# Optimization experiments

Measured on AMD Instinct MI355X. Metric: run time of the kernel, lower is better.

Reference implementation:

```python
import jax, jax.numpy as jnp
import numpy as np

# Straight-through sign binarization: forward -> {-1, +1}, backward -> identity
@jax.custom_vjp
def binarize(x):
    return jnp.where(x >= 0, jnp.ones_like(x), -jnp.ones_like(x))

def _bin_fwd(x):
    return binarize(x), None

def _bin_bwd(res, g):
    return (g,)

binarize.defvjp(_bin_fwd, _bin_bwd)

BATCH = 16384
IN_SIZE = 1025   # must be 2**n + 1
HIDDEN = 1025    # must be 2**n + 1

def setup_inputs() -> dict:
    key = jax.random.key(0)
    k0, k1, k2, k3 = jax.random.split(key, 4)
    # weight init scale per reset_parameters: sqrt(1.5/(in+out)) uniform
    s = float(np.sqrt(1.5 / (IN_SIZE + HIDDEN)))
    return {
        "x": jax.random.normal(k0, (BATCH, IN_SIZE), dtype=jnp.float32),
        "W0": jax.random.uniform(k1, (HIDDEN, IN_SIZE), jnp.float32, -s, s),
        "W1": jax.random.uniform(k2, (HIDDEN, HIDDEN), jnp.float32, -s, s),
        "W2": jax.random.uniform(k3, (1, HIDDEN), jnp.float32, -s, s),
    }

def reference(x, W0, W1, W2):
    # x: [B, IN_SIZE]; weights stored [out, in] (nn.Linear convention), no bias
    h = x.reshape(-1, IN_SIZE)
    for W in (W0, W1, W2):
        lin = h @ binarize(W).T          # float GEMM against +/-1 weights
        h = binarize(lin)                # sign activation
    # num_classes == 2 path: to_boolean maps {-1,+1} -> {0,1}, then squeeze
    out = (h + 1.0) * 0.5
    return out.squeeze(-1)               # [B]
```

## Files before the change

### kernel.cpp

```cpp
#include <hip/hip_runtime.h>
#include <cstdint>

typedef unsigned long long u64;
typedef unsigned short ushort_t;
typedef __attribute__((ext_vector_type(8))) short short8;
typedef __attribute__((ext_vector_type(4))) float f32x4;

#define B_TOTAL 16384
#define K_DIM   1025
#define O_DIM   1025
#define NWORDS  17
#define NKT     34
#define NFRAG   72
#define A_BYTES 8192
#define B_BYTES 73728
#define STEP_BYTES (A_BYTES + B_BYTES)
#define L23_ROWS 16

__device__ __forceinline__ ushort_t f2bf_rne(float f) {
  unsigned u = __float_as_uint(f);
  return (ushort_t)((u + 0x7fffu + ((u >> 16) & 1u)) >> 16);
}

__device__ __forceinline__ void gload16(const ushort_t* g, char* l) {
  __builtin_amdgcn_global_load_lds(
      (const __attribute__((address_space(1))) void*)g,
      (__attribute__((address_space(3))) void*)l, 16, 0, 0);
}

__global__ __launch_bounds__(256) void pack_all_kernel(const float* __restrict__ W0,
                                                       const float* __restrict__ W1,
                                                       const float* __restrict__ W2,
                                                       u64* __restrict__ w0b,
                                                       u64* __restrict__ w1b,
                                                       u64* __restrict__ w2b,
                                                       unsigned* cnt) {
  __shared__ unsigned char by[136];
  const int row = blockIdx.x, t = threadIdx.x;
  if (row == 0 && t == 0) *cnt = 0;
  const float* src; u64* dst; int o;
  if (row < O_DIM)           { src = W0; dst = w0b; o = row; }
  else if (row < 2 * O_DIM)  { src = W1; dst = w1b; o = row - O_DIM; }
  else                       { src = W2; dst = w2b; o = 0; }
  if (t < 136) {
    const float* wr = src + (size_t)o * K_DIM;
    unsigned m = 0;
#pragma unroll
    for (int j = 0; j < 8; ++j) {
      int k = t * 8 + j;
      bool pos = (k < K_DIM) ? (wr[k] >= 0.0f) : true;
      m |= (unsigned)pos << j;
    }
    by[t] = (unsigned char)m;
  }
  __syncthreads();
  if (t < NWORDS) {
    u64 word = 0;
#pragma unroll
    for (int q = 0; q < 8; ++q) word |= (u64)by[t * 8 + q] << (8 * q);
    dst[(size_t)o * NWORDS + t] = word;
  }
}

__global__ __launch_bounds__(256) void prep_sbf_kernel(const float* __restrict__ w0,
                                                       ushort_t* __restrict__ sbf) {
  const int t = threadIdx.x;
  const int f = blockIdx.x * 4 + (t >> 6);
  const int lane = t & 63;
  const int kt = f / NFRAG, nf = f % NFRAG;
  const int o = nf * 16 + (lane & 15);
  const int kbase = kt * 32 + (lane >> 4) * 8;
  short8 sv;
#pragma unroll
  for (int j = 0; j < 8; ++j) {
    int k = kbase + j;
    short v = 0;
    if (o < O_DIM && k < K_DIM)
      v = (short)((w0[(size_t)o * K_DIM + k] >= 0.0f) ? 0x3F80 : 0xBF80);
    sv[j] = v;
  }
  *(short8*)&sbf[(size_t)f * 512 + lane * 8] = sv;
}

__global__ __launch_bounds__(256) void prep_xf_kernel(const float* __restrict__ x,
                                                      ushort_t* __restrict__ xf,
                                                      float* __restrict__ errb) {
  const int p = blockIdx.x, t = threadIdx.x;
  const int mf = t >> 6, lane = t & 63;
  const int lr = lane & 15, lg = lane >> 4;
  const int brow = p * 64 + mf * 16 + lr;
  const float* xr = x + (size_t)brow * K_DIM;
  float s = 0.0f;
  for (int kt = 0; kt < NKT; ++kt) {
    const int kbase = kt * 32 + lg * 8;
    float v[8];
    if (kbase + 8 <= K_DIM) {
      float4 a = *(const float4*)(xr + kbase);
      float4 b = *(const float4*)(xr + kbase + 4);
      v[0]=a.x; v[1]=a.y; v[2]=a.z; v[3]=a.w; v[4]=b.x; v[5]=b.y; v[6]=b.z; v[7]=b.w;
    } else {
#pragma unroll
      for (int j = 0; j < 8; ++j) v[j] = (kbase + j < K_DIM) ? xr[kbase + j] : 0.0f;
    }
    short8 hi, lo;
#pragma unroll
    for (int j = 0; j < 8; ++j) {
      s += fabsf(v[j]);
      ushort_t h = f2bf_rne(v[j]);
      float hf = __uint_as_float((unsigned)h << 16);
      ushort_t l = f2bf_rne(v[j] - hf);
      hi[j] = (short)h; lo[j] = (short)l;
    }
    size_t base = ((size_t)(p * NKT + kt) * 8 + mf) * 512 + lane * 8;
    *(short8*)&xf[base] = hi;
    *(short8*)&xf[base + 4 * 512] = lo;
  }
  s += __shfl_xor(s, 16, 64);
  s += __shfl_xor(s, 32, 64);
  if (lg == 0) errb[brow] = s * (1.02f / 65536.0f) + 0.125f;
}

__global__ __launch_bounds__(512, 2) void l1_gemm_kernel(
    const ushort_t* __restrict__ xf, const ushort_t* __restrict__ sbf,
    const float* __restrict__ errb, u64* __restrict__ h1b,
    unsigned* __restrict__ cnt, unsigned* __restrict__ list, unsigned cap) {
  extern __shared__ char smem[];
  const int p = blockIdx.x;
  const int t = threadIdx.x;
  const int wave = t >> 6, lane = t & 63;
  const int lr = lane & 15, lg = lane >> 4;
  const int b0 = p * 64;
  const int obase = wave * 144;

  const ushort_t* gA = xf + (size_t)p * NKT * (A_BYTES / 2);

  f32x4 acc[4][9];
#pragma unroll
  for (int mf = 0; mf < 4; ++mf)
#pragma unroll
    for (int nfl = 0; nfl < 9; ++nfl)
#pragma unroll
      for (int c = 0; c < 4; ++c) acc[mf][nfl][c] = 0.0f;

#define STAGE(BUFI, KT)                                                        \
  {                                                                            \
    char* dbuf = smem + (BUFI) * STEP_BYTES;                                   \
    _Pragma("unroll")                                                          \
    for (int i = 0; i < 10; ++i) {                                             \
      int s = wave * 10 + i;                                                   \
      const ushort_t* g = (s < 8)                                              \
          ? gA + (KT) * (A_BYTES / 2) + s * 512 + lane * 8                     \
          : sbf + (size_t)(KT) * (B_BYTES / 2) + (s - 8) * 512 + lane * 8;     \
      gload16(g, dbuf + s * 1024);                                             \
    }                                                                          \
  }

  STAGE(0, 0);
  __syncthreads();
  int cur = 0;
  for (int kt = 0; kt < NKT; ++kt) {
    if (kt + 1 < NKT) STAGE(cur ^ 1, kt + 1);
    const ushort_t* A = (const ushort_t*)(smem + cur * STEP_BYTES);
    const ushort_t* Bf = A + A_BYTES / 2;
    short8 ah[4], al[4];
#pragma unroll
    for (int mf = 0; mf < 4; ++mf) {
      ah[mf] = *(const short8*)&A[mf * 512 + lane * 8];
      al[mf] = *(const short8*)&A[(4 + mf) * 512 + lane * 8];
    }
#pragma unroll
    for (int nfl = 0; nfl < 9; ++nfl) {
      short8 bv = *(const short8*)&Bf[(wave * 9 + nfl) * 512 + lane * 8];
#pragma unroll
      for (int mf = 0; mf < 4; ++mf) {
        acc[mf][nfl] = __builtin_amdgcn_mfma_f32_16x16x32_bf16(ah[mf], bv, acc[mf][nfl], 0, 0, 0);
        acc[mf][nfl] = __builtin_amdgcn_mfma_f32_16x16x32_bf16(al[mf], bv, acc[mf][nfl], 0, 0, 0);
      }
    }
    __syncthreads();
    cur ^= 1;
  }
#undef STAGE

  unsigned char* bits = (unsigned char*)smem;
  int* scan = (int*)(smem + 73728);

  float eb[4][4];
#pragma unroll
  for (int mf = 0; mf < 4; ++mf)
#pragma unroll
    for (int rg = 0; rg < 4; ++rg) eb[mf][rg] = errb[b0 + mf * 16 + lg * 4 + rg];

  int myCnt = 0;
#pragma unroll
  for (int mf = 0; mf < 4; ++mf)
#pragma unroll
    for (int nfl = 0; nfl < 9; ++nfl)
#pragma unroll
      for (int rg = 0; rg < 4; ++rg) {
        int bl = mf * 16 + lg * 4 + rg;
        int o  = obase + nfl * 16 + lr;
        float lin = acc[mf][nfl][rg];
        bits[bl * 1152 + o] = (lin >= 0.0f) ? 1u : 0u;
        myCnt += (int)((o < O_DIM) && (fabsf(lin) <= eb[mf][rg]));
      }

  int incl = myCnt;
#pragma unroll
  for (int d = 1; d < 64; d <<= 1) {
    int v = __shfl_up(incl, d, 64);
    if (lane >= d) incl += v;
  }
  if (lane == 63) scan[wave] = incl;
  __syncthreads();
  if (t == 0) {
    int run = 0;
#pragma unroll
    for (int i = 0; i < 8; ++i) { int c = scan[i]; scan[8 + i] = run; run += c; }
    scan[16] = (run > 0) ? (int)atomicAdd(cnt, (unsigned)run) : 0;
  }
  __syncthreads();

  {
    int off = scan[16] + scan[8 + wave] + incl - myCnt;
#pragma unroll
    for (int mf = 0; mf < 4; ++mf)
#pragma unroll
      for (int nfl = 0; nfl < 9; ++nfl)
#pragma unroll
        for (int rg = 0; rg < 4; ++rg) {
          int o = obase + nfl * 16 + lr;
          float lin = acc[mf][nfl][rg];
          if ((o < O_DIM) && (fabsf(lin) <= eb[mf][rg])) {
            int b = b0 + mf * 16 + lg * 4 + rg;
            unsigned abit = (lin >= 0.0f) ? 1u : 0u;
            if ((unsigned)off < cap)
              list[off] = ((unsigned)b << 12) | ((unsigned)o << 1) | abit;
            ++off;
          }
        }
  }

  for (int task = t; task < 64 * NWORDS; task += 512) {
    int row = task / NWORDS, w = task % NWORDS;
    u64 word = 0;
#pragma unroll
    for (int q = 0; q < 8; ++q) {
      u64 v = *(const u64*)&bits[row * 1152 + w * 64 + q * 8];
#pragma unroll
      for (int m = 0; m < 8; ++m)
        word |= ((v >> (8 * m)) & 1ull) << (q * 8 + m);
    }
    int rem = O_DIM - w * 64;
    if (rem < 64) word |= (~0ull << rem);
    h1b[(size_t)(b0 + row) * NWORDS + w] = word;
  }
}

__global__ void fixup_kernel(const float* __restrict__ x, const u64* __restrict__ w0b,
                             const unsigned* __restrict__ cnt, const unsigned* __restrict__ list,
                             unsigned cap, u64* __restrict__ h1b) {
  unsigned n = *cnt; if (n > cap) n = cap;
  for (unsigned i = blockIdx.x * blockDim.x + threadIdx.x; i < n;
       i += gridDim.x * blockDim.x) {
    unsigned en = list[i];
    int b = (int)(en >> 12), o = (int)((en >> 1) & 0x7ffu);
    unsigned abit = en & 1u;
    const float* xr = x + (size_t)b * K_DIM;
    const u64* wr = w0b + (size_t)o * NWORDS;
    float acc = 0.0f;
    for (int j = 0; j < 16; ++j) {
      u64 wd = wr[j];
#pragma unroll
      for (int m = 0; m < 64; ++m) {
        float v = xr[j * 64 + m];
        unsigned neg = ((unsigned)(wd >> m) & 1u) ^ 1u;
        acc += __uint_as_float(__float_as_uint(v) ^ (neg << 31));
      }
    }
    {
      u64 wd = wr[16];
      float v = xr[1024];
      unsigned neg = ((unsigned)wd & 1u) ^ 1u;
      acc += __uint_as_float(__float_as_uint(v) ^ (neg << 31));
    }
    unsigned nb = (acc >= 0.0f) ? 1u : 0u;
    if (nb != abit)
      atomicXor(&h1b[(size_t)b * NWORDS + (o >> 6)], 1ull << (o & 63));
  }
}

__global__ __launch_bounds__(256) void l2l3_kernel(const u64* __restrict__ h1b,
                                                   const u64* __restrict__ w1b,
                                                   const u64* __restrict__ w2b,
                                                   float* __restrict__ out) {
  __shared__ u64 hs[L23_ROWS][NWORDS];
  __shared__ u64 h2[L23_ROWS][NWORDS];
  const int bt = blockIdx.x;
  const int t = threadIdx.x;
  for (int i = t; i < L23_ROWS * NWORDS; i += 256)
    hs[i / NWORDS][i % NWORDS] = h1b[(size_t)(bt * L23_ROWS + i / NWORDS) * NWORDS + i % NWORDS];
  __syncthreads();

  const int w = t >> 6, l = t & 63;
  for (int oc = w; oc < NWORDS; oc += 4) {
    int o = oc * 64 + l;
    bool valid = (o < O_DIM);
    int orow = valid ? o : (O_DIM - 1);
    u64 wb[NWORDS];
#pragma unroll
    for (int j = 0; j < NWORDS; ++j) wb[j] = w1b[(size_t)orow * NWORDS + j];
    for (int b = 0; b < L23_ROWS; b += 2) {
      int p0 = 0, p1 = 0;
#pragma unroll
      for (int j = 0; j < NWORDS; ++j) {
        p0 += __popcll(hs[b + 0][j] ^ wb[j]);
        p1 += __popcll(hs[b + 1][j] ^ wb[j]);
      }
      u64 m0 = __ballot(valid ? (K_DIM - 2 * p0 >= 0) : true);
      u64 m1 = __ballot(valid ? (K_DIM - 2 * p1 >= 0) : true);
      if (l == 0) h2[b + 0][oc] = m0;
      if (l == 1) h2[b + 1][oc] = m1;
    }
  }
  __syncthreads();
  if (t < L23_ROWS) {
    int p = 0;
#pragma unroll
    for (int j = 0; j < NWORDS; ++j) p += __popcll(h2[t][j] ^ w2b[j]);
    out[bt * L23_ROWS + t] = ((K_DIM - 2 * p) >= 0) ? 1.0f : 0.0f;
  }
}

extern "C" void kernel_launch(void* const* d_in, const int* in_sizes, int n_in,
                              void* d_out, int out_size, void* d_ws, size_t ws_size,
                              hipStream_t stream) {
  const float* x  = (const float*)d_in[0];
  const float* W0 = (const float*)d_in[1];
  const float* W1 = (const float*)d_in[2];
  const float* W2 = (const float*)d_in[3];
  float* out = (float*)d_out;

  char* ws = (char*)d_ws;
  u64*      w0b  = (u64*)(ws);
  u64*      w1b  = (u64*)(ws + 139776);
  u64*      w2b  = (u64*)(ws + 279552);
  float*    errb = (float*)(ws + 279808);
  u64*      h1b  = (u64*)(ws + 345344);
  unsigned* cnt  = (unsigned*)(ws + 2573568);
  ushort_t* sbf  = (ushort_t*)(ws + 2573824);
  ushort_t* xf   = (ushort_t*)(ws + 5080576);
  unsigned* list = (unsigned*)(ws + 76383744);
  unsigned  cap  = (ws_size > 76383744 + 4) ? (unsigned)((ws_size - 76383744) / 4) : 0;

  static bool attr_set = false;
  if (!attr_set) {
    hipFuncSetAttribute((const void*)l1_gemm_kernel,
                        hipFuncAttributeMaxDynamicSharedMemorySize, 2 * STEP_BYTES);
    attr_set = true;
  }

  pack_all_kernel<<<2 * O_DIM + 1, 256, 0, stream>>>(W0, W1, W2, w0b, w1b, w2b, cnt);
  prep_sbf_kernel<<<NKT * NFRAG / 4, 256, 0, stream>>>(W0, sbf);
  prep_xf_kernel<<<B_TOTAL / 64, 256, 0, stream>>>(x, xf, errb);
  l1_gemm_kernel<<<B_TOTAL / 64, 512, 2 * STEP_BYTES, stream>>>(
      xf, sbf, errb, h1b, cnt, list, cap);
  fixup_kernel<<<1024, 256, 0, stream>>>(x, w0b, cnt, list, cap, h1b);
  l2l3_kernel<<<B_TOTAL / L23_ROWS, 256, 0, stream>>>(h1b, w1b, w2b, out);
}
```

Baseline: 185.5 us.

## Fuse fixup and binary layers 2-3 into the layer-1 GEMM kernel

The separate fixup and l2l3 kernels are merged into the tail of the layer-1 MFMA kernel. Each block now keeps its 64 rows of packed h1 bits in shared memory. It collects near-zero outputs into a shared-memory list using shared atomics instead of a block scan plus a global atomic. It recomputes those entries exactly against x, patches the bits with shared atomicXor, then runs the popcount layers 2 and 3 in place. This removes two launches, the global h1b round trip and the global flagged list. The cost is that correction work is serialized per block after the GEMM, with uneven wave balance, and the list is capped at 4096 entries per block, so any overflow silently skips corrections.

```diff
diff --git a/kernel.cpp b/kernel.cpp
--- a/kernel.cpp
+++ b/kernel.cpp
@@ -15,7 +15,7 @@
 #define A_BYTES 8192
 #define B_BYTES 73728
 #define STEP_BYTES (A_BYTES + B_BYTES)
-#define L23_ROWS 16
+#define FLAG_CAP 4096
 
 __device__ __forceinline__ ushort_t f2bf_rne(float f) {
   unsigned u = __float_as_uint(f);
@@ -33,11 +33,9 @@
                                                        const float* __restrict__ W2,
                                                        u64* __restrict__ w0b,
                                                        u64* __restrict__ w1b,
-                                                       u64* __restrict__ w2b,
-                                                       unsigned* cnt) {
+                                                       u64* __restrict__ w2b) {
   __shared__ unsigned char by[136];
   const int row = blockIdx.x, t = threadIdx.x;
-  if (row == 0 && t == 0) *cnt = 0;
   const float* src; u64* dst; int o;
   if (row < O_DIM)           { src = W0; dst = w0b; o = row; }
   else if (row < 2 * O_DIM)  { src = W1; dst = w1b; o = row - O_DIM; }
@@ -120,10 +118,11 @@
   if (lg == 0) errb[brow] = s * (1.02f / 65536.0f) + 0.125f;
 }
 
-__global__ __launch_bounds__(512, 2) void l1_gemm_kernel(
+__global__ __launch_bounds__(512, 2) void l1_fused_kernel(
     const ushort_t* __restrict__ xf, const ushort_t* __restrict__ sbf,
-    const float* __restrict__ errb, u64* __restrict__ h1b,
-    unsigned* __restrict__ cnt, unsigned* __restrict__ list, unsigned cap) {
+    const float* __restrict__ errb, const float* __restrict__ x,
+    const u64* __restrict__ w0b, const u64* __restrict__ w1b,
+    const u64* __restrict__ w2b, float* __restrict__ out) {
   extern __shared__ char smem[];
   const int p = blockIdx.x;
   const int t = threadIdx.x;
@@ -183,7 +182,14 @@
 #undef STAGE
 
   unsigned char* bits = (unsigned char*)smem;
-  int* scan = (int*)(smem + 73728);
+  u64*      hs   = (u64*)(smem + 73728);
+  u64*      h2   = (u64*)(smem + 82432);
+  unsigned* list = (unsigned*)(smem + 91136);
+  unsigned* lcnt = (unsigned*)(smem + 107520);
+  unsigned* hsw  = (unsigned*)hs;
+
+  if (t == 0) *lcnt = 0;
+  __syncthreads();
 
   float eb[4][4];
 #pragma unroll
@@ -191,7 +197,6 @@
 #pragma unroll
     for (int rg = 0; rg < 4; ++rg) eb[mf][rg] = errb[b0 + mf * 16 + lg * 4 + rg];
 
-  int myCnt = 0;
 #pragma unroll
   for (int mf = 0; mf < 4; ++mf)
 #pragma unroll
@@ -201,45 +206,15 @@
         int bl = mf * 16 + lg * 4 + rg;
         int o  = obase + nfl * 16 + lr;
         float lin = acc[mf][nfl][rg];
-        bits[bl * 1152 + o] = (lin >= 0.0f) ? 1u : 0u;
-        myCnt += (int)((o < O_DIM) && (fabsf(lin) <= eb[mf][rg]));
-      }
-
-  int incl = myCnt;
-#pragma unroll
-  for (int d = 1; d < 64; d <<= 1) {
-    int v = __shfl_up(incl, d, 64);
-    if (lane >= d) incl += v;
-  }
-  if (lane == 63) scan[wave] = incl;
-  __syncthreads();
-  if (t == 0) {
-    int run = 0;
-#pragma unroll
-    for (int i = 0; i < 8; ++i) { int c = scan[i]; scan[8 + i] = run; run += c; }
-    scan[16] = (run > 0) ? (int)atomicAdd(cnt, (unsigned)run) : 0;
-  }
-  __syncthreads();
-
-  {
-    int off = scan[16] + scan[8 + wave] + incl - myCnt;
-#pragma unroll
-    for (int mf = 0; mf < 4; ++mf)
-#pragma unroll
-      for (int nfl = 0; nfl < 9; ++nfl)
-#pragma unroll
-        for (int rg = 0; rg < 4; ++rg) {
-          int o = obase + nfl * 16 + lr;
-          float lin = acc[mf][nfl][rg];
-          if ((o < O_DIM) && (fabsf(lin) <= eb[mf][rg])) {
-            int b = b0 + mf * 16 + lg * 4 + rg;
-            unsigned abit = (lin >= 0.0f) ? 1u : 0u;
-            if ((unsigned)off < cap)
-              list[off] = ((unsigned)b << 12) | ((unsigned)o << 1) | abit;
-            ++off;
-          }
+        unsigned abit = (lin >= 0.0f) ? 1u : 0u;
+        bits[bl * 1152 + o] = (unsigned char)abit;
+        if ((o < O_DIM) && (fabsf(lin) <= eb[mf][rg])) {
+          unsigned idx = atomicAdd(lcnt, 1u);
+          if (idx < FLAG_CAP)
+            list[idx] = ((unsigned)bl << 12) | ((unsigned)o << 1) | abit;
         }
-  }
+      }
+  __syncthreads();
 
   for (int task = t; task < 64 * NWORDS; task += 512) {
     int row = task / NWORDS, w = task % NWORDS;
@@ -253,82 +228,71 @@
     }
     int rem = O_DIM - w * 64;
     if (rem < 64) word |= (~0ull << rem);
-    h1b[(size_t)(b0 + row) * NWORDS + w] = word;
-  }
-}
-
-__global__ void fixup_kernel(const float* __restrict__ x, const u64* __restrict__ w0b,
-                             const unsigned* __restrict__ cnt, const unsigned* __restrict__ list,
-                             unsigned cap, u64* __restrict__ h1b) {
-  unsigned n = *cnt; if (n > cap) n = cap;
-  for (unsigned i = blockIdx.x * blockDim.x + threadIdx.x; i < n;
-       i += gridDim.x * blockDim.x) {
-    unsigned en = list[i];
-    int b = (int)(en >> 12), o = (int)((en >> 1) & 0x7ffu);
-    unsigned abit = en & 1u;
-    const float* xr = x + (size_t)b * K_DIM;
-    const u64* wr = w0b + (size_t)o * NWORDS;
-    float acc = 0.0f;
-    for (int j = 0; j < 16; ++j) {
-      u64 wd = wr[j];
-#pragma unroll
-      for (int m = 0; m < 64; ++m) {
-        float v = xr[j * 64 + m];
-        unsigned neg = ((unsigned)(wd >> m) & 1u) ^ 1u;
-        acc += __uint_as_float(__float_as_uint(v) ^ (neg << 31));
-      }
-    }
-    {
-      u64 wd = wr[16];
-      float v = xr[1024];
-      unsigned neg = ((unsigned)wd & 1u) ^ 1u;
-      acc += __uint_as_float(__float_as_uint(v) ^ (neg << 31));
-    }
-    unsigned nb = (acc >= 0.0f) ? 1u : 0u;
-    if (nb != abit)
-      atomicXor(&h1b[(size_t)b * NWORDS + (o >> 6)], 1ull << (o & 63));
-  }
-}
-
-__global__ __launch_bounds__(256) void l2l3_kernel(const u64* __restrict__ h1b,
-                                                   const u64* __restrict__ w1b,
-                                                   const u64* __restrict__ w2b,
-                                                   float* __restrict__ out) {
-  __shared__ u64 hs[L23_ROWS][NWORDS];
-  __shared__ u64 h2[L23_ROWS][NWORDS];
-  const int bt = blockIdx.x;
-  const int t = threadIdx.x;
-  for (int i = t; i < L23_ROWS * NWORDS; i += 256)
-    hs[i / NWORDS][i % NWORDS] = h1b[(size_t)(bt * L23_ROWS + i / NWORDS) * NWORDS + i % NWORDS];
-  __syncthreads();
-
-  const int w = t >> 6, l = t & 63;
-  for (int oc = w; oc < NWORDS; oc += 4) {
-    int o = oc * 64 + l;
-    bool valid = (o < O_DIM);
-    int orow = valid ? o : (O_DIM - 1);
-    u64 wb[NWORDS];
-#pragma unroll
-    for (int j = 0; j < NWORDS; ++j) wb[j] = w1b[(size_t)orow * NWORDS + j];
-    for (int b = 0; b < L23_ROWS; b += 2) {
-      int p0 = 0, p1 = 0;
-#pragma unroll
-      for (int j = 0; j < NWORDS; ++j) {
-        p0 += __popcll(hs[b + 0][j] ^ wb[j]);
-        p1 += __popcll(hs[b + 1][j] ^ wb[j]);
-      }
-      u64 m0 = __ballot(valid ? (K_DIM - 2 * p0 >= 0) : true);
-      u64 m1 = __ballot(valid ? (K_DIM - 2 * p1 >= 0) : true);
-      if (l == 0) h2[b + 0][oc] = m0;
-      if (l == 1) h2[b + 1][oc] = m1;
-    }
-  }
-  __syncthreads();
-  if (t < L23_ROWS) {
-    int p = 0;
-#pragma unroll
-    for (int j = 0; j < NWORDS; ++j) p += __popcll(h2[t][j] ^ w2b[j]);
-    out[bt * L23_ROWS + t] = ((K_DIM - 2 * p) >= 0) ? 1.0f : 0.0f;
+    hs[row * NWORDS + w] = word;
+  }
+  __syncthreads();
+
+  {
+    unsigned n = *lcnt; if (n > FLAG_CAP) n = FLAG_CAP;
+    for (unsigned i = t; i < n; i += 512) {
+      unsigned en = list[i];
+      int bl = (int)(en >> 12), o = (int)((en >> 1) & 0x7ffu);
+      unsigned abit = en & 1u;
+      const float* xr = x + (size_t)(b0 + bl) * K_DIM;
+      const u64* wr = w0b + (size_t)o * NWORDS;
+      float a = 0.0f;
+      for (int j = 0; j < 16; ++j) {
+        u64 wd = wr[j];
+#pragma unroll
+        for (int m = 0; m < 64; ++m) {
+          float v = xr[j * 64 + m];
+          unsigned neg = ((unsigned)(wd >> m) & 1u) ^ 1u;
+          a += __uint_as_float(__float_as_uint(v) ^ (neg << 31));
+        }
+      }
+      {
+        u64 wd = wr[16];
+        float v = xr[1024];
+        unsigned neg = ((unsigned)wd & 1u) ^ 1u;
+        a += __uint_as_float(__float_as_uint(v) ^ (neg << 31));
+      }
+      unsigned nb = (a >= 0.0f) ? 1u : 0u;
+      if (nb != abit)
+        atomicXor(&hsw[bl * 34 + (o >> 5)], 1u << (o & 31));
+    }
+  }
+  __syncthreads();
+
+  {
+    const int wv = t >> 6, l = t & 63;
+    for (int oc = wv; oc < NWORDS; oc += 8) {
+      int o = oc * 64 + l;
+      bool valid = (o < O_DIM);
+      int orow = valid ? o : (O_DIM - 1);
+      u64 wb[NWORDS];
+#pragma unroll
+      for (int j = 0; j < NWORDS; ++j) wb[j] = w1b[(size_t)orow * NWORDS + j];
+      for (int b = 0; b < 64; b += 2) {
+        int p0 = 0, p1 = 0;
+#pragma unroll
+        for (int j = 0; j < NWORDS; ++j) {
+          p0 += __popcll(hs[(b + 0) * NWORDS + j] ^ wb[j]);
+          p1 += __popcll(hs[(b + 1) * NWORDS + j] ^ wb[j]);
+        }
+        u64 m0 = __ballot(valid ? (K_DIM - 2 * p0 >= 0) : true);
+        u64 m1 = __ballot(valid ? (K_DIM - 2 * p1 >= 0) : true);
+        if (l == 0) h2[(b + 0) * NWORDS + oc] = m0;
+        if (l == 1) h2[(b + 1) * NWORDS + oc] = m1;
+      }
+    }
+  }
+  __syncthreads();
+
+  if (t < 64) {
+    int pc = 0;
+#pragma unroll
+    for (int j = 0; j < NWORDS; ++j) pc += __popcll(h2[t * NWORDS + j] ^ w2b[j]);
+    out[b0 + t] = ((K_DIM - 2 * pc) >= 0) ? 1.0f : 0.0f;
   }
 }
 
@@ -346,25 +310,19 @@
   u64*      w1b  = (u64*)(ws + 139776);
   u64*      w2b  = (u64*)(ws + 279552);
   float*    errb = (float*)(ws + 279808);
-  u64*      h1b  = (u64*)(ws + 345344);
-  unsigned* cnt  = (unsigned*)(ws + 2573568);
-  ushort_t* sbf  = (ushort_t*)(ws + 2573824);
-  ushort_t* xf   = (ushort_t*)(ws + 5080576);
-  unsigned* list = (unsigned*)(ws + 76383744);
-  unsigned  cap  = (ws_size > 76383744 + 4) ? (unsigned)((ws_size - 76383744) / 4) : 0;
+  ushort_t* sbf  = (ushort_t*)(ws + 345344);
+  ushort_t* xf   = (ushort_t*)(ws + 2852096);
 
   static bool attr_set = false;
   if (!attr_set) {
-    hipFuncSetAttribute((const void*)l1_gemm_kernel,
+    hipFuncSetAttribute((const void*)l1_fused_kernel,
                         hipFuncAttributeMaxDynamicSharedMemorySize, 2 * STEP_BYTES);
     attr_set = true;
   }
 
-  pack_all_kernel<<<2 * O_DIM + 1, 256, 0, stream>>>(W0, W1, W2, w0b, w1b, w2b, cnt);
+  pack_all_kernel<<<2 * O_DIM + 1, 256, 0, stream>>>(W0, W1, W2, w0b, w1b, w2b);
   prep_sbf_kernel<<<NKT * NFRAG / 4, 256, 0, stream>>>(W0, sbf);
   prep_xf_kernel<<<B_TOTAL / 64, 256, 0, stream>>>(x, xf, errb);
-  l1_gemm_kernel<<<B_TOTAL / 64, 512, 2 * STEP_BYTES, stream>>>(
-      xf, sbf, errb, h1b, cnt, list, cap);
-  fixup_kernel<<<1024, 256, 0, stream>>>(x, w0b, cnt, list, cap, h1b);
-  l2l3_kernel<<<B_TOTAL / L23_ROWS, 256, 0, stream>>>(h1b, w1b, w2b, out);
-}
+  l1_fused_kernel<<<B_TOTAL / 64, 512, 2 * STEP_BYTES, stream>>>(
+      xf, sbf, errb, x, w0b, w1b, w2b, out);
+}
```

Result: faster. 180.7 us (-2.6%).
